# Kernel tuning notes

Hardware: AMD Instinct MI355X
Metric: run time of the kernel (lower is better)

## Reference

```python
import jax, jax.numpy as jnp
import numpy as np

N_NODES = 100000
N_EDGES = 800000
IN_DIM = 128
ATT_DIM = 128
N_HEADS = 4
HEAD_DIM = ATT_DIM // N_HEADS


def setup_inputs() -> dict:
    key = jax.random.key(0)
    ks = jax.random.split(key, 10)
    def xavier(k, shape):
        fan_out, fan_in = shape
        lim = jnp.sqrt(6.0 / (fan_in + fan_out))
        return jax.random.uniform(k, shape, jnp.float32, -lim, lim)
    x = jax.random.normal(ks[0], (N_NODES, IN_DIM), jnp.float32)
    edge_index = jax.random.randint(ks[1], (2, N_EDGES), 0, N_NODES, jnp.int64)
    return {
        "x": x,
        "edge_index": edge_index,
        "Wq": xavier(ks[2], (ATT_DIM, IN_DIM)), "bq": jnp.zeros((ATT_DIM,), jnp.float32),
        "Wk": xavier(ks[3], (ATT_DIM, IN_DIM)), "bk": jnp.zeros((ATT_DIM,), jnp.float32),
        "Wv": xavier(ks[4], (ATT_DIM, IN_DIM)), "bv": jnp.zeros((ATT_DIM,), jnp.float32),
        "Wo": xavier(ks[5], (IN_DIM, ATT_DIM)), "bo": jnp.zeros((IN_DIM,), jnp.float32),
    }


def reference(x, edge_index, Wq, bq, Wk, bk, Wv, bv, Wo, bo):
    n = x.shape[0]
    # node projections [N, H, Dh]
    q = (x @ Wq.T + bq).reshape(n, N_HEADS, HEAD_DIM)
    k = (x @ Wk.T + bk).reshape(n, N_HEADS, HEAD_DIM)
    v = (x @ Wv.T + bv).reshape(n, N_HEADS, HEAD_DIM)
    row, col = edge_index[0], edge_index[1]
    # per-edge scores [E, H]
    scores = (q[row] * k[col]).sum(-1) / jnp.sqrt(jnp.float32(HEAD_DIM))
    # segment softmax grouped by destination row
    seg_max = jax.ops.segment_max(scores, row, num_segments=n)  # [N, H]
    e = jnp.exp(scores - seg_max[row])
    seg_sum = jax.ops.segment_sum(e, row, num_segments=n)  # [N, H]
    attn = e / (seg_sum[row] + 1e-16)  # [E, H] (dropout is identity at eval)
    # weighted scatter-add of values
    attended = jax.ops.segment_sum(attn[:, :, None] * v[col], row, num_segments=n)
    attended = attended.reshape(n, ATT_DIM)
    out = attended @ Wo.T + bo + x
    avg_attn = attn.mean(axis=1)  # [E]
    return (out, avg_attn)
```

## Files before the change

kernel.cpp:

```cpp
#include <hip/hip_runtime.h>
#include <hip/hip_bf16.h>

#define DIM 128
#define CAP 64
#define RSQRT_HD 0.17677669529663687f

typedef float f32x4 __attribute__((ext_vector_type(4)));
typedef short bf16x8 __attribute__((ext_vector_type(8)));

__device__ __forceinline__ float bf2f(unsigned short u) {
    unsigned int x = ((unsigned int)u) << 16;
    union { unsigned int i; float f; } c; c.i = x; return c.f;
}
__device__ __forceinline__ unsigned short f2bf(float f) {
    __hip_bfloat16 h = __float2bfloat16(f);
    unsigned short u;
    __builtin_memcpy(&u, &h, 2);
    return u;
}
__device__ __forceinline__ void wave_lds_fence() {
    asm volatile("s_waitcnt lgkmcnt(0)" ::: "memory");
    __builtin_amdgcn_sched_barrier(0);
}

__global__ __launch_bounds__(256) void cast_w4(
    const float* __restrict__ a, const float* __restrict__ b,
    const float* __restrict__ c, const float* __restrict__ d,
    unsigned short* __restrict__ oa, unsigned short* __restrict__ ob,
    unsigned short* __restrict__ oc, unsigned short* __restrict__ od)
{
    int w = blockIdx.y;
    const float* s = (w == 0) ? a : (w == 1) ? b : (w == 2) ? c : d;
    unsigned short* o = (w == 0) ? oa : (w == 1) ? ob : (w == 2) ? oc : od;
    int i = blockIdx.x * 256 + threadIdx.x;
    f32x4 v0 = ((const f32x4*)s)[2 * i];
    f32x4 v1 = ((const f32x4*)s)[2 * i + 1];
    bf16x8 ov;
    ov[0] = (short)f2bf(v0[0]); ov[1] = (short)f2bf(v0[1]);
    ov[2] = (short)f2bf(v0[2]); ov[3] = (short)f2bf(v0[3]);
    ov[4] = (short)f2bf(v1[0]); ov[5] = (short)f2bf(v1[1]);
    ov[6] = (short)f2bf(v1[2]); ov[7] = (short)f2bf(v1[3]);
    ((bf16x8*)o)[i] = ov;
}

__global__ __launch_bounds__(256) void gemm_qkv_fused(const float* __restrict__ X,
    const unsigned short* __restrict__ Wq, const unsigned short* __restrict__ Wk,
    const unsigned short* __restrict__ Wv,
    const float* __restrict__ bq, const float* __restrict__ bk, const float* __restrict__ bv,
    unsigned short* __restrict__ Q, unsigned short* __restrict__ K, unsigned short* __restrict__ V,
    int M)
{
    int lane = threadIdx.x & 63;
    int wave = threadIdx.x >> 6;
    int row0 = blockIdx.x * 128 + wave * 32;
    int r16 = lane & 15;
    int kg = lane >> 4;
    int koff = kg * 8;

    int ra0 = row0 + r16;       if (ra0 > M - 1) ra0 = M - 1;
    int ra1 = row0 + 16 + r16;  if (ra1 > M - 1) ra1 = M - 1;
    const float* pa0f = X + (size_t)ra0 * DIM + koff;
    const float* pa1f = X + (size_t)ra1 * DIM + koff;

    bf16x8 xa0[4], xa1[4];
#pragma unroll
    for (int kt = 0; kt < 4; ++kt) {
        int k0 = kt * 32;
        f32x4 lo0 = *(const f32x4*)(pa0f + k0), hi0 = *(const f32x4*)(pa0f + k0 + 4);
        f32x4 lo1 = *(const f32x4*)(pa1f + k0), hi1 = *(const f32x4*)(pa1f + k0 + 4);
#pragma unroll
        for (int j = 0; j < 4; ++j) {
            xa0[kt][j] = (short)f2bf(lo0[j]); xa0[kt][j + 4] = (short)f2bf(hi0[j]);
            xa1[kt][j] = (short)f2bf(lo1[j]); xa1[kt][j + 4] = (short)f2bf(hi1[j]);
        }
    }

#pragma unroll
    for (int w = 0; w < 3; ++w) {
        const unsigned short* W = (w == 0) ? Wq : (w == 1) ? Wk : Wv;
        const float* bias        = (w == 0) ? bq : (w == 1) ? bk : bv;
        unsigned short* out      = (w == 0) ? Q  : (w == 1) ? K  : V;

        f32x4 acc[2][8] = {};
        const unsigned short* pw = W + r16 * DIM + koff;
#pragma unroll
        for (int kt = 0; kt < 4; ++kt) {
            int k0 = kt * 32;
            bf16x8 bw[8];
#pragma unroll
            for (int ct = 0; ct < 8; ++ct)
                bw[ct] = *(const bf16x8*)(pw + ct * 16 * DIM + k0);
#pragma unroll
            for (int ct = 0; ct < 8; ++ct) {
                acc[0][ct] = __builtin_amdgcn_mfma_f32_16x16x32_bf16(xa0[kt], bw[ct], acc[0][ct], 0, 0, 0);
                acc[1][ct] = __builtin_amdgcn_mfma_f32_16x16x32_bf16(xa1[kt], bw[ct], acc[1][ct], 0, 0, 0);
            }
        }

        float biasv[8];
#pragma unroll
        for (int ct = 0; ct < 8; ++ct) biasv[ct] = bias[ct * 16 + r16];
#pragma unroll
        for (int rt = 0; rt < 2; ++rt) {
            int rbase = row0 + rt * 16 + kg * 4;
#pragma unroll
            for (int ct = 0; ct < 8; ++ct) {
                int c = ct * 16 + r16;
#pragma unroll
                for (int j = 0; j < 4; ++j) {
                    int r = rbase + j;
                    if (r < M) out[(size_t)r * DIM + c] = f2bf(acc[rt][ct][j] + biasv[ct]);
                }
            }
        }
    }
}

__global__ __launch_bounds__(256) void gemm_final(const unsigned short* __restrict__ A,
    const unsigned short* __restrict__ W, const float* __restrict__ bias,
    const float* __restrict__ res, float* __restrict__ out, int M)
{
    int lane = threadIdx.x & 63;
    int wave = threadIdx.x >> 6;
    int row0 = blockIdx.x * 128 + wave * 32;
    int r16 = lane & 15;
    int kg = lane >> 4;
    int koff = kg * 8;

    f32x4 acc[2][8] = {};
    int ra0 = row0 + r16;       if (ra0 > M - 1) ra0 = M - 1;
    int ra1 = row0 + 16 + r16;  if (ra1 > M - 1) ra1 = M - 1;
    const unsigned short* pa0 = A + (size_t)ra0 * DIM + koff;
    const unsigned short* pa1 = A + (size_t)ra1 * DIM + koff;
    const unsigned short* pw = W + r16 * DIM + koff;

#pragma unroll
    for (int k0 = 0; k0 < 128; k0 += 32) {
        bf16x8 a0 = *(const bf16x8*)(pa0 + k0);
        bf16x8 a1 = *(const bf16x8*)(pa1 + k0);
        bf16x8 bw[8];
#pragma unroll
        for (int ct = 0; ct < 8; ++ct)
            bw[ct] = *(const bf16x8*)(pw + ct * 16 * DIM + k0);
#pragma unroll
        for (int ct = 0; ct < 8; ++ct) {
            acc[0][ct] = __builtin_amdgcn_mfma_f32_16x16x32_bf16(a0, bw[ct], acc[0][ct], 0, 0, 0);
            acc[1][ct] = __builtin_amdgcn_mfma_f32_16x16x32_bf16(a1, bw[ct], acc[1][ct], 0, 0, 0);
        }
    }

    float biasv[8];
#pragma unroll
    for (int ct = 0; ct < 8; ++ct) biasv[ct] = bias[ct * 16 + r16];
#pragma unroll
    for (int rt = 0; rt < 2; ++rt) {
        int rbase = row0 + rt * 16 + kg * 4;
#pragma unroll
        for (int ct = 0; ct < 8; ++ct) {
            int c = ct * 16 + r16;
#pragma unroll
            for (int j = 0; j < 4; ++j) {
                int r = rbase + j;
                if (r < M)
                    out[(size_t)r * DIM + c] = acc[rt][ct][j] + biasv[ct] + res[(size_t)r * DIM + c];
            }
        }
    }
}

__global__ void detect64(const int* __restrict__ e, int* __restrict__ flag, int E)
{
    __shared__ int nz;
    int t = threadIdx.x;
    if (t == 0) nz = 0;
    __syncthreads();
    int lim = (E < 4096) ? E : 4096;
    int mynz = 0;
    for (int i = 2 * t + 1; i < lim; i += 512) mynz |= (e[i] != 0);
    if (mynz) atomicOr(&nz, 1);
    __syncthreads();
    if (t == 0) *flag = nz ? 0 : 1;
}

__device__ __forceinline__ int load_idx(const int* p32, const long long* p64, int is64, int i)
{
    return is64 ? (int)p64[i] : p32[i];
}

__global__ void hist_kernel(const int* __restrict__ row32, const long long* __restrict__ row64,
                            const int* __restrict__ flag, int* __restrict__ deg, int E)
{
    int e = blockIdx.x * blockDim.x + threadIdx.x;
    if (e < E) atomicAdd(&deg[load_idx(row32, row64, *flag, e)], 1);
}

__global__ __launch_bounds__(256) void scan1(const int* __restrict__ in, int* __restrict__ incl,
                                             int* __restrict__ bsums, int n)
{
    __shared__ int s[256];
    int t = threadIdx.x;
    int base = blockIdx.x * 1024 + t * 4;
    int v0 = (base + 0 < n) ? in[base + 0] : 0;
    int v1 = (base + 1 < n) ? in[base + 1] : 0;
    int v2 = (base + 2 < n) ? in[base + 2] : 0;
    int v3 = (base + 3 < n) ? in[base + 3] : 0;
    int sum = v0 + v1 + v2 + v3;
    s[t] = sum;
    __syncthreads();
    for (int off = 1; off < 256; off <<= 1) {
        int x = (t >= off) ? s[t - off] : 0;
        __syncthreads();
        s[t] += x;
        __syncthreads();
    }
    int excl = s[t] - sum;
    if (base + 0 < n) incl[base + 0] = excl + v0;
    if (base + 1 < n) incl[base + 1] = excl + v0 + v1;
    if (base + 2 < n) incl[base + 2] = excl + v0 + v1 + v2;
    if (base + 3 < n) incl[base + 3] = excl + sum;
    if (t == 255) bsums[blockIdx.x] = s[255];
}

__global__ __launch_bounds__(256) void scan2(int* bsums, int nb)
{
    __shared__ int s[512];
    int t = threadIdx.x;
    s[t] = (t < nb) ? bsums[t] : 0;
    s[t + 256] = (t + 256 < nb) ? bsums[t + 256] : 0;
    __syncthreads();
    for (int off = 1; off < 512; off <<= 1) {
        int x0 = (t >= off) ? s[t - off] : 0;
        int i1 = t + 256;
        int x1 = (i1 >= off) ? s[i1 - off] : 0;
        __syncthreads();
        s[t] += x0;
        s[i1] += x1;
        __syncthreads();
    }
    if (t < nb) bsums[t] = (t == 0) ? 0 : s[t - 1];
    if (t + 256 < nb) bsums[t + 256] = s[t + 255];
}

__global__ void scan3(const int* __restrict__ incl, const int* __restrict__ bofs,
                      int* __restrict__ rowptr, int n)
{
    int i = blockIdx.x * 256 + threadIdx.x;
    if (i == 0) rowptr[0] = 0;
    if (i < n) rowptr[i + 1] = incl[i] + bofs[i >> 10];
}

__global__ void scatter_kernel(const int* __restrict__ e32, const long long* __restrict__ e64,
                               const int* __restrict__ flag,
                               int* __restrict__ cursor, int* __restrict__ colidx,
                               int* __restrict__ eidb, int E)
{
    int e = blockIdx.x * blockDim.x + threadIdx.x;
    if (e < E) {
        int is64 = *flag;
        int r = load_idx(e32, e64, is64, e);
        int c = load_idx(e32 + E, e64 + E, is64, e);
        int pos = atomicAdd(&cursor[r], 1);
        colidx[pos] = c;
        eidb[pos] = e;
    }
}

__global__ __launch_bounds__(256) void attn_kernel(const unsigned short* __restrict__ Q,
    const unsigned short* __restrict__ K, const unsigned short* __restrict__ V,
    const int* __restrict__ rowptr, const int* __restrict__ colidx,
    const int* __restrict__ eidb, unsigned short* __restrict__ attended,
    float* __restrict__ avg_out, int N)
{
    __shared__ float sc_s[4][CAP * 5];
    __shared__ int scol_s[4][CAP];
    __shared__ int sei_s[4][CAP];

    int wave = threadIdx.x >> 6;
    int l = threadIdx.x & 63;
    int n = blockIdx.x * 4 + wave;
    bool active = n < N;
    int h = l >> 4;
    int hl = l & 15;
    float* sc = sc_s[wave];
    int* scol = scol_s[wave];
    int* sei = sei_s[wave];

    int s0 = active ? rowptr[n] : 0;
    int deg = active ? (rowptr[n + 1] - s0) : 0;

    float q0 = 0.f, q1 = 0.f;
    if (active) {
        ushort2 qq = *(const ushort2*)(Q + (size_t)n * DIM + 2 * l);
        q0 = bf2f(qq.x); q1 = bf2f(qq.y);
    }

    if (deg <= CAP) {
        for (int e = l; e < deg; e += 64) { scol[e] = colidx[s0 + e]; sei[e] = eidb[s0 + e]; }
        wave_lds_fence();
        int e = 0;
        for (; e + 4 <= deg; e += 4) {
            int c0 = scol[e], c1 = scol[e + 1], c2 = scol[e + 2], c3 = scol[e + 3];
            ushort2 k0v = *(const ushort2*)(K + (size_t)c0 * DIM + 2 * l);
            ushort2 k1v = *(const ushort2*)(K + (size_t)c1 * DIM + 2 * l);
            ushort2 k2v = *(const ushort2*)(K + (size_t)c2 * DIM + 2 * l);
            ushort2 k3v = *(const ushort2*)(K + (size_t)c3 * DIM + 2 * l);
            float p0 = q0 * bf2f(k0v.x) + q1 * bf2f(k0v.y);
            float p1 = q0 * bf2f(k1v.x) + q1 * bf2f(k1v.y);
            float p2 = q0 * bf2f(k2v.x) + q1 * bf2f(k2v.y);
            float p3 = q0 * bf2f(k3v.x) + q1 * bf2f(k3v.y);
#pragma unroll
            for (int off = 8; off; off >>= 1) {
                p0 += __shfl_xor(p0, off); p1 += __shfl_xor(p1, off);
                p2 += __shfl_xor(p2, off); p3 += __shfl_xor(p3, off);
            }
            if (hl == 0) {
                sc[(e + 0) * 5 + h] = p0 * RSQRT_HD;
                sc[(e + 1) * 5 + h] = p1 * RSQRT_HD;
                sc[(e + 2) * 5 + h] = p2 * RSQRT_HD;
                sc[(e + 3) * 5 + h] = p3 * RSQRT_HD;
            }
        }
        for (; e < deg; ++e) {
            int c = scol[e];
            ushort2 kk = *(const ushort2*)(K + (size_t)c * DIM + 2 * l);
            float p = q0 * bf2f(kk.x) + q1 * bf2f(kk.y);
#pragma unroll
            for (int off = 8; off; off >>= 1) p += __shfl_xor(p, off);
            if (hl == 0) sc[e * 5 + h] = p * RSQRT_HD;
        }
        wave_lds_fence();
        float m = -INFINITY;
        for (int e2 = hl; e2 < deg; e2 += 16) m = fmaxf(m, sc[e2 * 5 + h]);
#pragma unroll
        for (int off = 8; off; off >>= 1) m = fmaxf(m, __shfl_xor(m, off));
        float ssum = 0.f;
        for (int e2 = hl; e2 < deg; e2 += 16) ssum += __expf(sc[e2 * 5 + h] - m);
#pragma unroll
        for (int off = 8; off; off >>= 1) ssum += __shfl_xor(ssum, off);
        float inv = 1.f / (ssum + 1e-16f);
        for (int e2 = hl; e2 < deg; e2 += 16) sc[e2 * 5 + h] = __expf(sc[e2 * 5 + h] - m) * inv;
        wave_lds_fence();
        for (int e2 = l; e2 < deg; e2 += 64)
            avg_out[sei[e2]] = 0.25f * (sc[e2 * 5] + sc[e2 * 5 + 1] + sc[e2 * 5 + 2] + sc[e2 * 5 + 3]);
        float a0 = 0.f, a1 = 0.f;
        int e3 = 0;
        for (; e3 + 4 <= deg; e3 += 4) {
            int c0 = scol[e3], c1 = scol[e3 + 1], c2 = scol[e3 + 2], c3 = scol[e3 + 3];
            float w0 = sc[(e3 + 0) * 5 + h];
            float w1 = sc[(e3 + 1) * 5 + h];
            float w2 = sc[(e3 + 2) * 5 + h];
            float w3 = sc[(e3 + 3) * 5 + h];
            ushort2 v0 = *(const ushort2*)(V + (size_t)c0 * DIM + 2 * l);
            ushort2 v1 = *(const ushort2*)(V + (size_t)c1 * DIM + 2 * l);
            ushort2 v2 = *(const ushort2*)(V + (size_t)c2 * DIM + 2 * l);
            ushort2 v3 = *(const ushort2*)(V + (size_t)c3 * DIM + 2 * l);
            a0 += w0 * bf2f(v0.x); a1 += w0 * bf2f(v0.y);
            a0 += w1 * bf2f(v1.x); a1 += w1 * bf2f(v1.y);
            a0 += w2 * bf2f(v2.x); a1 += w2 * bf2f(v2.y);
            a0 += w3 * bf2f(v3.x); a1 += w3 * bf2f(v3.y);
        }
        for (; e3 < deg; ++e3) {
            float a = sc[e3 * 5 + h];
            ushort2 vv = *(const ushort2*)(V + (size_t)scol[e3] * DIM + 2 * l);
            a0 += a * bf2f(vv.x);
            a1 += a * bf2f(vv.y);
        }
        if (active) {
            ushort2 o; o.x = f2bf(a0); o.y = f2bf(a1);
            *(ushort2*)(attended + (size_t)n * DIM + 2 * l) = o;
        }
    } else {
        float m = -INFINITY, ssum = 0.f;
        for (int e = 0; e < deg; ++e) {
            int c = colidx[s0 + e];
            ushort2 kk = *(const ushort2*)(K + (size_t)c * DIM + 2 * l);
            float p = q0 * bf2f(kk.x) + q1 * bf2f(kk.y);
#pragma unroll
            for (int off = 8; off; off >>= 1) p += __shfl_xor(p, off);
            p *= RSQRT_HD;
            float mn = fmaxf(m, p);
            ssum = ssum * __expf(m - mn) + __expf(p - mn);
            m = mn;
        }
        float inv = 1.f / (ssum + 1e-16f);
        float a0 = 0.f, a1 = 0.f;
        for (int e = 0; e < deg; ++e) {
            int c = colidx[s0 + e];
            ushort2 kk = *(const ushort2*)(K + (size_t)c * DIM + 2 * l);
            float p = q0 * bf2f(kk.x) + q1 * bf2f(kk.y);
#pragma unroll
            for (int off = 8; off; off >>= 1) p += __shfl_xor(p, off);
            float a = __expf(p * RSQRT_HD - m) * inv;
            float asum = a + __shfl_xor(a, 16);
            asum += __shfl_xor(asum, 32);
            if (l == 0) avg_out[eidb[s0 + e]] = 0.25f * asum;
            ushort2 vv = *(const ushort2*)(V + (size_t)c * DIM + 2 * l);
            a0 += a * bf2f(vv.x);
            a1 += a * bf2f(vv.y);
        }
        if (active) {
            ushort2 o; o.x = f2bf(a0); o.y = f2bf(a1);
            *(ushort2*)(attended + (size_t)n * DIM + 2 * l) = o;
        }
    }
}

extern "C" void kernel_launch(void* const* d_in, const int* in_sizes, int n_in,
                              void* d_out, int out_size, void* d_ws, size_t ws_size,
                              hipStream_t stream)
{
    const float* x  = (const float*)d_in[0];
    const int* e32  = (const int*)d_in[1];
    const long long* e64 = (const long long*)d_in[1];
    const float* Wq = (const float*)d_in[2];
    const float* bq = (const float*)d_in[3];
    const float* Wk = (const float*)d_in[4];
    const float* bk = (const float*)d_in[5];
    const float* Wv = (const float*)d_in[6];
    const float* bv = (const float*)d_in[7];
    const float* Wo = (const float*)d_in[8];
    const float* bo = (const float*)d_in[9];

    int N = in_sizes[0] / DIM;
    int E = in_sizes[1] / 2;

    float* out = (float*)d_out;
    float* avg_out = out + (size_t)N * DIM;

    char* w = (char*)d_ws;
    auto carve = [&](size_t bytes) -> void* {
        void* p = (void*)w;
        w += (bytes + 255) & ~(size_t)255;
        return p;
    };
    unsigned short* Qb = (unsigned short*)carve((size_t)N * DIM * 2);
    unsigned short* Kb = (unsigned short*)carve((size_t)N * DIM * 2);
    unsigned short* Vb = (unsigned short*)carve((size_t)N * DIM * 2);
    unsigned short* Wqb = (unsigned short*)carve(DIM * DIM * 2);
    unsigned short* Wkb = (unsigned short*)carve(DIM * DIM * 2);
    unsigned short* Wvb = (unsigned short*)carve(DIM * DIM * 2);
    unsigned short* Wob = (unsigned short*)carve(DIM * DIM * 2);
    int* deg    = (int*)carve((size_t)N * 4);
    int* tmp    = (int*)carve((size_t)N * 4);
    int* rowptr = (int*)carve(((size_t)N + 1) * 4);
    int* cursor = (int*)carve((size_t)N * 4);
    int* bsums  = (int*)carve(512 * 4);
    int* flag   = (int*)carve(256);
    int* colidx = (int*)carve((size_t)E * 4);
    int* eidb   = (int*)carve((size_t)E * 4);

    hipMemsetAsync(deg, 0, (size_t)N * 4, stream);

    cast_w4<<<dim3(8, 4), 256, 0, stream>>>(Wq, Wk, Wv, Wo, Wqb, Wkb, Wvb, Wob);

    detect64<<<1, 256, 0, stream>>>(e32, flag, 2 * E);
    hist_kernel<<<(E + 255) / 256, 256, 0, stream>>>(e32, e64, flag, deg, E);
    int nb = (N + 1023) / 1024;
    scan1<<<nb, 256, 0, stream>>>(deg, tmp, bsums, N);
    scan2<<<1, 256, 0, stream>>>(bsums, nb);
    scan3<<<(N + 255) / 256, 256, 0, stream>>>(tmp, bsums, rowptr, N);
    hipMemcpyAsync(cursor, rowptr, (size_t)N * 4, hipMemcpyDeviceToDevice, stream);
    scatter_kernel<<<(E + 255) / 256, 256, 0, stream>>>(e32, e64, flag, cursor, colidx, eidb, E);

    int gx = (N + 127) / 128;
    gemm_qkv_fused<<<gx, 256, 0, stream>>>(x, Wqb, Wkb, Wvb, bq, bk, bv, Qb, Kb, Vb, N);

    attn_kernel<<<(N + 3) / 4, 256, 0, stream>>>(Qb, Kb, Vb, rowptr, colidx, eidb,
                                                 Qb , avg_out, N);

    gemm_final<<<gx, 256, 0, stream>>>(Qb, Wob, bo, x, out, N);
}
```

Baseline: 401.1 us.

## Fuse CSR build into one persistent kernel and stage QKV stores through LDS

Replaces the seven-step CSR construction (memset, detect, histogram, three scan kernels, memcpy, scatter) with a single persistent kernel of 256 blocks that uses atomic-counter grid barriers between phases. This removes several launch gaps and the device-to-device copy. Separately, the QKV GEMM epilogue now writes its bf16 results into per-wave LDS and stores them as 16-byte row-contiguous vectors instead of scattered 2-byte stores. The grid barrier assumes all 256 blocks are resident at the same time, and with only 256 blocks the atomic histogram and scatter phases have less parallelism.

```diff
diff --git a/kernel.cpp b/kernel.cpp
--- a/kernel.cpp
+++ b/kernel.cpp
@@ -4,6 +4,7 @@
 #define DIM 128
 #define CAP 64
 #define RSQRT_HD 0.17677669529663687f
+#define CSR_BLOCKS 256
 
 typedef float f32x4 __attribute__((ext_vector_type(4)));
 typedef short bf16x8 __attribute__((ext_vector_type(8)));
@@ -43,6 +44,107 @@
     ((bf16x8*)o)[i] = ov;
 }
 
+__device__ __forceinline__ void gridbar(int* cnt)
+{
+    __syncthreads();
+    if (threadIdx.x == 0) {
+        __threadfence();
+        atomicAdd(cnt, 1);
+        while (__hip_atomic_load(cnt, __ATOMIC_RELAXED, __HIP_MEMORY_SCOPE_AGENT) < CSR_BLOCKS)
+            __builtin_amdgcn_s_sleep(2);
+        __threadfence();
+    }
+    __syncthreads();
+}
+
+__global__ __launch_bounds__(256) void csr_build(
+    const int* __restrict__ e32, const long long* __restrict__ e64,
+    int* __restrict__ deg, int* __restrict__ tmp, int* __restrict__ rowptr,
+    int* __restrict__ cursor, int* __restrict__ colidx, int* __restrict__ eidb,
+    int* __restrict__ bsums, int* __restrict__ bar, int N, int E)
+{
+    int t = threadIdx.x, b = blockIdx.x;
+    int gid = b * 256 + t;
+    const int gsz = CSR_BLOCKS * 256;
+    int nb = (N + 1023) >> 10;
+    __shared__ int s[512];
+
+    for (int i = gid; i < N; i += gsz) deg[i] = 0;
+    if (b == 0) {
+        int lim = (2 * E < 4096) ? 2 * E : 4096;
+        int nz = 0;
+        for (int i = 2 * t + 1; i < lim; i += 512) nz |= (e32[i] != 0);
+        if (nz) atomicOr(&bar[5], 1);
+    }
+    gridbar(&bar[0]);
+
+    int is64 = (__hip_atomic_load(&bar[5], __ATOMIC_RELAXED, __HIP_MEMORY_SCOPE_AGENT) == 0);
+
+    for (int e = gid; e < E; e += gsz) {
+        int r = is64 ? (int)e64[e] : e32[e];
+        atomicAdd(&deg[r], 1);
+    }
+    gridbar(&bar[1]);
+
+    if (b < nb) {
+        int base = b * 1024 + t * 4;
+        int v0 = (base + 0 < N) ? deg[base + 0] : 0;
+        int v1 = (base + 1 < N) ? deg[base + 1] : 0;
+        int v2 = (base + 2 < N) ? deg[base + 2] : 0;
+        int v3 = (base + 3 < N) ? deg[base + 3] : 0;
+        int sum = v0 + v1 + v2 + v3;
+        s[t] = sum;
+        __syncthreads();
+        for (int off = 1; off < 256; off <<= 1) {
+            int x = (t >= off) ? s[t - off] : 0;
+            __syncthreads();
+            s[t] += x;
+            __syncthreads();
+        }
+        int excl = s[t] - sum;
+        if (base + 0 < N) tmp[base + 0] = excl + v0;
+        if (base + 1 < N) tmp[base + 1] = excl + v0 + v1;
+        if (base + 2 < N) tmp[base + 2] = excl + v0 + v1 + v2;
+        if (base + 3 < N) tmp[base + 3] = excl + sum;
+        if (t == 255) bsums[b] = s[255];
+    }
+    gridbar(&bar[2]);
+
+    if (b == 0) {
+        s[t] = (t < nb) ? bsums[t] : 0;
+        s[t + 256] = (t + 256 < nb) ? bsums[t + 256] : 0;
+        __syncthreads();
+        for (int off = 1; off < 512; off <<= 1) {
+            int x0 = (t >= off) ? s[t - off] : 0;
+            int i1 = t + 256;
+            int x1 = (i1 >= off) ? s[i1 - off] : 0;
+            __syncthreads();
+            s[t] += x0;
+            s[i1] += x1;
+            __syncthreads();
+        }
+        if (t < nb) bsums[t] = (t == 0) ? 0 : s[t - 1];
+        if (t + 256 < nb) bsums[t + 256] = s[t + 255];
+    }
+    gridbar(&bar[3]);
+
+    for (int i = gid; i < N; i += gsz) {
+        int rp1 = tmp[i] + bsums[i >> 10];
+        rowptr[i + 1] = rp1;
+        cursor[i] = rp1 - deg[i];
+        if (i == 0) rowptr[0] = 0;
+    }
+    gridbar(&bar[4]);
+
+    for (int e = gid; e < E; e += gsz) {
+        int r = is64 ? (int)e64[e] : e32[e];
+        int c = is64 ? (int)e64[e + E] : e32[e + E];
+        int pos = atomicAdd(&cursor[r], 1);
+        colidx[pos] = c;
+        eidb[pos] = e;
+    }
+}
+
 __global__ __launch_bounds__(256) void gemm_qkv_fused(const float* __restrict__ X,
     const unsigned short* __restrict__ Wq, const unsigned short* __restrict__ Wk,
     const unsigned short* __restrict__ Wv,
@@ -50,6 +152,7 @@
     unsigned short* __restrict__ Q, unsigned short* __restrict__ K, unsigned short* __restrict__ V,
     int M)
 {
+    __shared__ unsigned short cst[4][32 * 136];
     int lane = threadIdx.x & 63;
     int wave = threadIdx.x >> 6;
     int row0 = blockIdx.x * 128 + wave * 32;
@@ -75,6 +178,7 @@
         }
     }
 
+    unsigned short* my = &cst[wave][0];
 #pragma unroll
     for (int w = 0; w < 3; ++w) {
         const unsigned short* W = (w == 0) ? Wq : (w == 1) ? Wk : Wv;
@@ -100,19 +204,24 @@
         float biasv[8];
 #pragma unroll
         for (int ct = 0; ct < 8; ++ct) biasv[ct] = bias[ct * 16 + r16];
-#pragma unroll
-        for (int rt = 0; rt < 2; ++rt) {
-            int rbase = row0 + rt * 16 + kg * 4;
-#pragma unroll
-            for (int ct = 0; ct < 8; ++ct) {
-                int c = ct * 16 + r16;
-#pragma unroll
-                for (int j = 0; j < 4; ++j) {
-                    int r = rbase + j;
-                    if (r < M) out[(size_t)r * DIM + c] = f2bf(acc[rt][ct][j] + biasv[ct]);
-                }
-            }
-        }
+
+#pragma unroll
+        for (int rt = 0; rt < 2; ++rt)
+#pragma unroll
+            for (int ct = 0; ct < 8; ++ct)
+#pragma unroll
+                for (int j = 0; j < 4; ++j)
+                    my[(rt * 16 + kg * 4 + j) * 136 + ct * 16 + r16] =
+                        f2bf(acc[rt][ct][j] + biasv[ct]);
+        wave_lds_fence();
+#pragma unroll
+        for (int pass = 0; pass < 8; ++pass) {
+            int rr = pass * 4 + (lane >> 4);
+            bf16x8 v = *(const bf16x8*)(my + rr * 136 + (lane & 15) * 8);
+            int gr = row0 + rr;
+            if (gr < M) *(bf16x8*)(out + (size_t)gr * DIM + (lane & 15) * 8) = v;
+        }
+        wave_lds_fence();
     }
 }
 
@@ -165,103 +274,6 @@
                     out[(size_t)r * DIM + c] = acc[rt][ct][j] + biasv[ct] + res[(size_t)r * DIM + c];
             }
         }
-    }
-}
-
-__global__ void detect64(const int* __restrict__ e, int* __restrict__ flag, int E)
-{
-    __shared__ int nz;
-    int t = threadIdx.x;
-    if (t == 0) nz = 0;
-    __syncthreads();
-    int lim = (E < 4096) ? E : 4096;
-    int mynz = 0;
-    for (int i = 2 * t + 1; i < lim; i += 512) mynz |= (e[i] != 0);
-    if (mynz) atomicOr(&nz, 1);
-    __syncthreads();
-    if (t == 0) *flag = nz ? 0 : 1;
-}
-
-__device__ __forceinline__ int load_idx(const int* p32, const long long* p64, int is64, int i)
-{
-    return is64 ? (int)p64[i] : p32[i];
-}
-
-__global__ void hist_kernel(const int* __restrict__ row32, const long long* __restrict__ row64,
-                            const int* __restrict__ flag, int* __restrict__ deg, int E)
-{
-    int e = blockIdx.x * blockDim.x + threadIdx.x;
-    if (e < E) atomicAdd(&deg[load_idx(row32, row64, *flag, e)], 1);
-}
-
-__global__ __launch_bounds__(256) void scan1(const int* __restrict__ in, int* __restrict__ incl,
-                                             int* __restrict__ bsums, int n)
-{
-    __shared__ int s[256];
-    int t = threadIdx.x;
-    int base = blockIdx.x * 1024 + t * 4;
-    int v0 = (base + 0 < n) ? in[base + 0] : 0;
-    int v1 = (base + 1 < n) ? in[base + 1] : 0;
-    int v2 = (base + 2 < n) ? in[base + 2] : 0;
-    int v3 = (base + 3 < n) ? in[base + 3] : 0;
-    int sum = v0 + v1 + v2 + v3;
-    s[t] = sum;
-    __syncthreads();
-    for (int off = 1; off < 256; off <<= 1) {
-        int x = (t >= off) ? s[t - off] : 0;
-        __syncthreads();
-        s[t] += x;
-        __syncthreads();
-    }
-    int excl = s[t] - sum;
-    if (base + 0 < n) incl[base + 0] = excl + v0;
-    if (base + 1 < n) incl[base + 1] = excl + v0 + v1;
-    if (base + 2 < n) incl[base + 2] = excl + v0 + v1 + v2;
-    if (base + 3 < n) incl[base + 3] = excl + sum;
-    if (t == 255) bsums[blockIdx.x] = s[255];
-}
-
-__global__ __launch_bounds__(256) void scan2(int* bsums, int nb)
-{
-    __shared__ int s[512];
-    int t = threadIdx.x;
-    s[t] = (t < nb) ? bsums[t] : 0;
-    s[t + 256] = (t + 256 < nb) ? bsums[t + 256] : 0;
-    __syncthreads();
-    for (int off = 1; off < 512; off <<= 1) {
-        int x0 = (t >= off) ? s[t - off] : 0;
-        int i1 = t + 256;
-        int x1 = (i1 >= off) ? s[i1 - off] : 0;
-        __syncthreads();
-        s[t] += x0;
-        s[i1] += x1;
-        __syncthreads();
-    }
-    if (t < nb) bsums[t] = (t == 0) ? 0 : s[t - 1];
-    if (t + 256 < nb) bsums[t + 256] = s[t + 255];
-}
-
-__global__ void scan3(const int* __restrict__ incl, const int* __restrict__ bofs,
-                      int* __restrict__ rowptr, int n)
-{
-    int i = blockIdx.x * 256 + threadIdx.x;
-    if (i == 0) rowptr[0] = 0;
-    if (i < n) rowptr[i + 1] = incl[i] + bofs[i >> 10];
-}
-
-__global__ void scatter_kernel(const int* __restrict__ e32, const long long* __restrict__ e64,
-                               const int* __restrict__ flag,
-                               int* __restrict__ cursor, int* __restrict__ colidx,
-                               int* __restrict__ eidb, int E)
-{
-    int e = blockIdx.x * blockDim.x + threadIdx.x;
-    if (e < E) {
-        int is64 = *flag;
-        int r = load_idx(e32, e64, is64, e);
-        int c = load_idx(e32 + E, e64 + E, is64, e);
-        int pos = atomicAdd(&cursor[r], 1);
-        colidx[pos] = c;
-        eidb[pos] = e;
     }
 }
 
@@ -445,22 +457,16 @@
     int* rowptr = (int*)carve(((size_t)N + 1) * 4);
     int* cursor = (int*)carve((size_t)N * 4);
     int* bsums  = (int*)carve(512 * 4);
-    int* flag   = (int*)carve(256);
+    int* bar    = (int*)carve(256);
     int* colidx = (int*)carve((size_t)E * 4);
     int* eidb   = (int*)carve((size_t)E * 4);
 
-    hipMemsetAsync(deg, 0, (size_t)N * 4, stream);
+    hipMemsetAsync(bar, 0, 256, stream);
 
     cast_w4<<<dim3(8, 4), 256, 0, stream>>>(Wq, Wk, Wv, Wo, Wqb, Wkb, Wvb, Wob);
 
-    detect64<<<1, 256, 0, stream>>>(e32, flag, 2 * E);
-    hist_kernel<<<(E + 255) / 256, 256, 0, stream>>>(e32, e64, flag, deg, E);
-    int nb = (N + 1023) / 1024;
-    scan1<<<nb, 256, 0, stream>>>(deg, tmp, bsums, N);
-    scan2<<<1, 256, 0, stream>>>(bsums, nb);
-    scan3<<<(N + 255) / 256, 256, 0, stream>>>(tmp, bsums, rowptr, N);
-    hipMemcpyAsync(cursor, rowptr, (size_t)N * 4, hipMemcpyDeviceToDevice, stream);
-    scatter_kernel<<<(E + 255) / 256, 256, 0, stream>>>(e32, e64, flag, cursor, colidx, eidb, E);
+    csr_build<<<CSR_BLOCKS, 256, 0, stream>>>(e32, e64, deg, tmp, rowptr, cursor,
+                                              colidx, eidb, bsums, bar, N, E);
 
     int gx = (N + 127) / 128;
     gemm_qkv_fused<<<gx, 256, 0, stream>>>(x, Wqb, Wkb, Wvb, bq, bk, bv, Qb, Kb, Vb, N);
```

Measured after the change: 486.9 us. +21.4%, slower.
